# Performance work log

Hardware: AMD Instinct MI355X
Metric: run time of the kernel (lower is better)

## Reference

```python
import jax, jax.numpy as jnp
import numpy as np

THETA = 10000.0


def _rope(x, pos, theta):
    # x: [..., S, d_k] with d_k even; pos: [..., S] int positions
    d_k = x.shape[-1]
    inv_freq = 1.0 / (theta ** (jnp.arange(0, d_k, 2, dtype=jnp.float32) / d_k))  # [d_k/2]
    ang = pos[..., None].astype(jnp.float32) * inv_freq  # [..., S, d_k/2]
    cos, sin = jnp.cos(ang), jnp.sin(ang)
    x1 = x[..., 0::2]
    x2 = x[..., 1::2]
    r1 = x1 * cos - x2 * sin
    r2 = x1 * sin + x2 * cos
    # interleave back to [..., S, d_k]
    return jnp.stack([r1, r2], axis=-1).reshape(x.shape)


def setup_inputs() -> dict:
    key = jax.random.key(0)
    ks = jax.random.split(key, 5)
    B, S, D = 2, 2048, 1024
    scale = 0.02
    return {
        "in_features": jax.random.normal(ks[0], (B, S, D), dtype=jnp.float32),
        "q_proj": jax.random.normal(ks[1], (D, D), dtype=jnp.float32) * scale,
        "k_proj": jax.random.normal(ks[2], (D, D), dtype=jnp.float32) * scale,
        "v_proj": jax.random.normal(ks[3], (D, D), dtype=jnp.float32) * scale,
        "o_proj": jax.random.normal(ks[4], (D, D), dtype=jnp.float32) * scale,
    }


def reference(in_features, q_proj, k_proj, v_proj, o_proj):
    B, S, D = in_features.shape
    H = 16
    d_k = D // H
    pos = jnp.arange(S)  # broadcast over batch/heads

    def split_heads(x):  # [B,S,D] -> [B,H,S,d_k]
        return x.reshape(B, S, H, d_k).transpose(0, 2, 1, 3)

    Q = split_heads(in_features @ q_proj.T)
    K = split_heads(in_features @ k_proj.T)
    V = split_heads(in_features @ v_proj.T)

    Q = _rope(Q, pos, THETA)
    K = _rope(K, pos, THETA)

    scores = jnp.einsum("bhqd,bhkd->bhqk", Q, K) / jnp.sqrt(jnp.float32(d_k))
    causal = jnp.tril(jnp.ones((S, S), dtype=bool))
    scores = jnp.where(causal, scores, jnp.finfo(scores.dtype).min)
    attn = jax.nn.softmax(scores, axis=-1)
    out = jnp.einsum("bhqk,bhkd->bhqd", attn, V)  # [B,H,S,d_k]
    out = out.transpose(0, 2, 1, 3).reshape(B, S, D)
    return out @ o_proj.T
```

## Files before the change

kernel.cpp:

```cpp
#include <hip/hip_runtime.h>
#include <hip/hip_bf16.h>
#include <math.h>

#define Bdim 2
#define Sdim 2048
#define Ddim 1024
#define Hdim 16
#define DKdim 64
#define Mrows 4096

typedef __attribute__((ext_vector_type(8))) short bf16x8;
typedef __attribute__((ext_vector_type(4))) short short4v;
typedef __attribute__((ext_vector_type(4))) float f32x4;
typedef __attribute__((ext_vector_type(2))) unsigned int uint2v;

#define LOG2E_DIV8 0.18033688011112042f
#define NLOG2TH_64 0.20762050593046016f

__device__ __forceinline__ short f2bf(float f) {
  unsigned int x = __float_as_uint(f);
  x += 0x7fffu + ((x >> 16) & 1u);
  return (short)(x >> 16);
}

__device__ __forceinline__ float fast_exp2(float x) {
#if __has_builtin(__builtin_amdgcn_exp2f)
  return __builtin_amdgcn_exp2f(x);
#else
  return exp2f(x);
#endif
}

__device__ __forceinline__ unsigned int pack_bf2(float lo, float hi) {
  unsigned int r;
  asm("v_cvt_pk_bf16_f32 %0, %1, %2" : "=v"(r) : "v"(lo), "v"(hi));
  return r;
}

__device__ __forceinline__ void gl2lds16(const void* g, void* l) {
  __builtin_amdgcn_global_load_lds(
      (const __attribute__((address_space(1))) void*)g,
      (__attribute__((address_space(3))) void*)l, 16, 0, 0);
}

__global__ void cvt_kernel(const float* __restrict__ src, short* __restrict__ dst, int n) {
  int i = (blockIdx.x * blockDim.x + threadIdx.x) * 4;
  if (i + 3 < n) {
    float4 v = *(const float4*)(src + i);
    short4v o;
    o.x = f2bf(v.x); o.y = f2bf(v.y); o.z = f2bf(v.z); o.w = f2bf(v.w);
    *(short4v*)(dst + i) = o;
  }
}

__global__ void rope_tab_kernel(float2* __restrict__ T) {
  int idx = blockIdx.x * blockDim.x + threadIdx.x;
  int s = idx >> 5, f = idx & 31;
  float inv = exp2f(-NLOG2TH_64 * (float)(2 * f));
  float ang = (float)s * inv;
  float sn, cs;
  sincosf(ang, &sn, &cs);
  T[idx] = make_float2(sn, cs);
}

template<int MODE>
__global__ __launch_bounds__(256) void gemm_bt(
    const short* __restrict__ A, const short* __restrict__ Bw,
    float* __restrict__ Cf,
    short* __restrict__ Qout, short* __restrict__ Kout, short* __restrict__ Vout,
    const float2* __restrict__ RT,
    int Ndim, int Kdim)
{
  __shared__ __align__(16) short smem[17408];
  short (*st)[136] = (short(*)[136])smem;
  char* smemb = (char*)smem;

  const int tid  = threadIdx.x;
  const int lane = tid & 63;
  const int wid  = tid >> 6;
  const int wr = wid >> 1, wc = wid & 1;
  const int tile_m = blockIdx.x * 128;
  const int tile_n = blockIdx.y * 128;
  const int lrow = lane & 15;
  const int kgrp = lane >> 4;

  const int r0 = tid >> 2;
  const int sc = (tid & 3) * 8;
  const int lA0 = wid * 1024;
  const int lA1 = 4096  + wid * 1024;
  const int lB0 = 8192  + wid * 1024;
  const int lB1 = 12288 + wid * 1024;
  const short* gA0 = A  + (size_t)(tile_m + r0)      * Kdim + sc;
  const short* gA1 = A  + (size_t)(tile_m + r0 + 64) * Kdim + sc;
  const short* gB0 = Bw + (size_t)(tile_n + r0)      * Kdim + sc;
  const short* gB1 = Bw + (size_t)(tile_n + r0 + 64) * Kdim + sc;

  f32x4 acc[4][4];
#pragma unroll
  for (int i = 0; i < 4; i++)
#pragma unroll
    for (int j = 0; j < 4; j++) acc[i][j] = (f32x4)0.0f;

  for (int k0 = 0; k0 < Kdim; k0 += 32) {
    __syncthreads();
    gl2lds16(gA0 + k0, smemb + lA0);
    gl2lds16(gA1 + k0, smemb + lA1);
    gl2lds16(gB0 + k0, smemb + lB0);
    gl2lds16(gB1 + k0, smemb + lB1);
    __syncthreads();
    bf16x8 af[4], bfr[4];
#pragma unroll
    for (int i = 0; i < 4; i++)
      af[i]  = *(const bf16x8*)&smem[(wr*64 + i*16 + lrow)*32 + kgrp*8];
#pragma unroll
    for (int j = 0; j < 4; j++)
      bfr[j] = *(const bf16x8*)&smem[4096 + (wc*64 + j*16 + lrow)*32 + kgrp*8];
#pragma unroll
    for (int i = 0; i < 4; i++)
#pragma unroll
      for (int j = 0; j < 4; j++)
        acc[i][j] = __builtin_amdgcn_mfma_f32_16x16x32_bf16(af[i], bfr[j], acc[i][j], 0, 0, 0);
  }

  if (MODE == 0) {
#pragma unroll
    for (int i = 0; i < 4; i++)
#pragma unroll
      for (int j = 0; j < 4; j++)
#pragma unroll
        for (int r = 0; r < 4; r++) {
          int mr = tile_m + wr*64 + i*16 + kgrp*4 + r;
          int nc = tile_n + wc*64 + j*16 + lrow;
          Cf[(size_t)mr * Ndim + nc] = acc[i][j][r];
        }
  } else {
    const int sel = tile_n >> 10;
    __syncthreads();
#pragma unroll
    for (int i = 0; i < 4; i++)
#pragma unroll
      for (int j = 0; j < 4; j++)
#pragma unroll
        for (int r = 0; r < 4; r++) {
          float val   = acc[i][j][r];
          float other = __shfl_xor(val, 1, 64);
          int row = wr*64 + i*16 + kgrp*4 + r;
          int col = wc*64 + j*16 + lrow;
          short bv;
          if (sel == 2) {
            bv = f2bf(val);
          } else {
            int c = col & 63;
            int s = (tile_m + row) & 2047;
            float2 t = RT[(s << 5) + (c >> 1)];
            float rot = ((c & 1) == 0) ? (val * t.y - other * t.x)
                                       : (other * t.x + val * t.y);
            if (sel == 0) rot *= LOG2E_DIV8;
            bv = f2bf(rot);
          }
          st[row][col] = bv;
        }
    __syncthreads();
    if (sel < 2) {
      short* Out = (sel == 0) ? Qout : Kout;
#pragma unroll
      for (int p = 0; p < 8; p++) {
        int row = p*16 + (tid >> 4);
        int col = (tid & 15) * 8;
        bf16x8 v = *(const bf16x8*)&st[row][col];
        int mr = tile_m + row; int b = mr >> 11, s = mr & 2047;
        int nc = tile_n + col; int nn = nc & 1023;
        int h = nn >> 6, c = nn & 63;
        *(bf16x8*)&Out[((size_t)((b*Hdim + h)*Sdim + s))*DKdim + c] = v;
      }
    } else {
#pragma unroll
      for (int p = 0; p < 8; p++) {
        int col = p*16 + (tid >> 4);
        int sl  = (tid & 15) * 8;
        bf16x8 v;
#pragma unroll
        for (int e = 0; e < 8; e++) v[e] = st[sl + e][col];
        int nc = tile_n + col; int nn = nc & 1023;
        int h = nn >> 6, c = nn & 63;
        int m0 = tile_m + sl; int b = m0 >> 11, s0 = m0 & 2047;
        *(bf16x8*)&Vout[((size_t)((b*Hdim + h)*DKdim + c))*Sdim + s0] = v;
      }
    }
  }
}

__global__ __launch_bounds__(256, 2) void attn_kernel(
    const short* __restrict__ Q, const short* __restrict__ K,
    const short* __restrict__ Vt, short* __restrict__ O)
{
  const int bh = blockIdx.y;
  const int qt = (bh & 16) ? (int)blockIdx.x : (15 - (int)blockIdx.x);
  const int bq0 = qt * 128;
  const int tid  = threadIdx.x;
  const int wave = tid >> 6;
  const int lane = tid & 63;
  const int lrow = lane & 15, kgrp = lane >> 4;
  const short* Qb = Q  + (size_t)bh * Sdim * DKdim;
  const short* Kb = K  + (size_t)bh * Sdim * DKdim;
  const short* Vb = Vt + (size_t)bh * DKdim * Sdim;

  __shared__ __align__(16) char Kl[2][16384];
  __shared__ __align__(16) char Vl[2][16384];
  __shared__ __align__(16) char lPb[16384];

  const int q0w   = bq0 + wave*32;
  const int NT_w  = (q0w >> 6) + 1;
  const int NTP   = qt + 1;
  const int swz   = (lrow & 7) << 4;
  const int rowbase = wave*4096 + lrow*128;

  const int ldsoff = wave*4096 +  0;

  bf16x8 qf[2][2];
#pragma unroll
  for (int t = 0; t < 2; t++) {
    qf[t][0] = *(const bf16x8*)&Qb[(q0w + t*16 + lrow) * DKdim + kgrp*8];
    qf[t][1] = *(const bf16x8*)&Qb[(q0w + t*16 + lrow) * DKdim + 32 + kgrp*8];
  }

  f32x4 o[2][4];
  float psum[2] = {0.0f, 0.0f};
#pragma unroll
  for (int t = 0; t < 2; t++)
#pragma unroll
    for (int n = 0; n < 4; n++) o[t][n] = (f32x4)0.0f;

#pragma unroll
  for (int q = 0; q < 4; q++) {
    int c = wave*256 + q*64 + lane;
    int krow = c >> 3, kc16 = c & 7;
    gl2lds16((const char*)Kb + (size_t)krow * 128 + ((kc16*16) ^ ((krow & 7) << 4)),
             (char*)Kl[0] + ldsoff + q*1024);
    int vrow = c >> 4, vc16 = c & 15;
    gl2lds16((const char*)Vb + (size_t)vrow * (Sdim*2) + ((vc16*16) ^ ((vrow & 7) << 4)),
             (char*)Vl[0] + ldsoff + q*1024);
  }
  __syncthreads();

  int cur = 0;
  for (int it = 0; it < NTP; ++it) {
    const bool havenext = (it + 1 < NTP);
    if (havenext) {
      const int nkv = (it + 1) << 7;
      char* Kd = (char*)Kl[cur ^ 1] + ldsoff;
      char* Vd = (char*)Vl[cur ^ 1] + ldsoff;
#pragma unroll
      for (int q = 0; q < 4; q++) {
        int c = wave*256 + q*64 + lane;
        int krow = c >> 3, kc16 = c & 7;
        gl2lds16((const char*)Kb + (size_t)(nkv + krow) * 128 + ((kc16*16) ^ ((krow & 7) << 4)),
                 Kd + q*1024);
        int vrow = c >> 4, vc16 = c & 15;
        gl2lds16((const char*)Vb + (size_t)vrow * (Sdim*2) + nkv*2 + ((vc16*16) ^ ((vrow & 7) << 4)),
                 Vd + q*1024);
      }
    }
#pragma unroll
    for (int stt = 0; stt < 2; ++stt) {
      const int j = 2*it + stt;
      if (j < NT_w) {
        const int kv0 = j << 6;
        const char* Kc = Kl[cur] + stt*8192;
        const char* Vc = Vl[cur];
        const int vbo = stt*128;
        f32x4 sacc[2][4];
#pragma unroll
        for (int t = 0; t < 2; t++)
#pragma unroll
          for (int nch = 0; nch < 4; nch++) sacc[t][nch] = (f32x4)0.0f;
        __builtin_amdgcn_s_setprio(1);
#pragma unroll
        for (int nch = 0; nch < 4; nch++) {
          int rb = (nch*16 + lrow)*128;
          bf16x8 kf0 = *(const bf16x8*)(Kc + rb + ((kgrp*16) ^ swz));
          bf16x8 kf1 = *(const bf16x8*)(Kc + rb + ((kgrp*16 + 64) ^ swz));
          sacc[0][nch] = __builtin_amdgcn_mfma_f32_16x16x32_bf16(kf0, qf[0][0], sacc[0][nch], 0, 0, 0);
          sacc[0][nch] = __builtin_amdgcn_mfma_f32_16x16x32_bf16(kf1, qf[0][1], sacc[0][nch], 0, 0, 0);
          sacc[1][nch] = __builtin_amdgcn_mfma_f32_16x16x32_bf16(kf0, qf[1][0], sacc[1][nch], 0, 0, 0);
          sacc[1][nch] = __builtin_amdgcn_mfma_f32_16x16x32_bf16(kf1, qf[1][1], sacc[1][nch], 0, 0, 0);
        }
        __builtin_amdgcn_s_setprio(0);
        const bool diag = (j == NT_w - 1);
#pragma unroll
        for (int t = 0; t < 2; t++) {
          const int q_abs = q0w + t*16 + lrow;
#pragma unroll
          for (int nch = 0; nch < 4; nch++) {
            const int kbase = kv0 + nch*16 + kgrp*4;
            float p[4];
#pragma unroll
            for (int r = 0; r < 4; r++) {
              float e = fast_exp2(sacc[t][nch][r]);
              p[r] = (diag && (kbase + r > q_abs)) ? 0.0f : e;
            }
            psum[t] += (p[0] + p[1]) + (p[2] + p[3]);
            uint2v w;
            w.x = pack_bf2(p[0], p[1]);
            w.y = pack_bf2(p[2], p[3]);
            *(uint2v*)(lPb + rowbase + t*2048 + ((nch*32 + kgrp*8) ^ swz)) = w;
          }
        }
        asm volatile("s_waitcnt lgkmcnt(0)" ::: "memory");
        __builtin_amdgcn_sched_barrier(0);
        bf16x8 pa[2][2];
#pragma unroll
        for (int t = 0; t < 2; t++)
#pragma unroll
          for (int h = 0; h < 2; h++)
            pa[t][h] = *(const bf16x8*)(lPb + rowbase + t*2048 + ((h*64 + kgrp*16) ^ swz));
        __builtin_amdgcn_s_setprio(1);
#pragma unroll
        for (int n = 0; n < 4; n++) {
          int rb = (n*16 + lrow)*256 + vbo;
          bf16x8 vf0 = *(const bf16x8*)(Vc + rb + ((kgrp*16) ^ swz));
          bf16x8 vf1 = *(const bf16x8*)(Vc + rb + ((kgrp*16 + 64) ^ swz));
          o[0][n] = __builtin_amdgcn_mfma_f32_16x16x32_bf16(pa[0][0], vf0, o[0][n], 0, 0, 0);
          o[0][n] = __builtin_amdgcn_mfma_f32_16x16x32_bf16(pa[0][1], vf1, o[0][n], 0, 0, 0);
          o[1][n] = __builtin_amdgcn_mfma_f32_16x16x32_bf16(pa[1][0], vf0, o[1][n], 0, 0, 0);
          o[1][n] = __builtin_amdgcn_mfma_f32_16x16x32_bf16(pa[1][1], vf1, o[1][n], 0, 0, 0);
        }
        __builtin_amdgcn_s_setprio(0);
      }
    }
    __syncthreads();
    cur ^= 1;
  }

  float vt[2];
#pragma unroll
  for (int t = 0; t < 2; t++) {
    float v = psum[t];
    v += __shfl_xor(v, 16, 64);
    v += __shfl_xor(v, 32, 64);
    vt[t] = v;
  }
  const int hh = bh & 15, b = bh >> 4;
#pragma unroll
  for (int t = 0; t < 2; t++)
#pragma unroll
    for (int r = 0; r < 4; r++) {
      float rs = __frcp_rn(__shfl(vt[t], kgrp*4 + r, 64));
      int row = q0w + t*16 + kgrp*4 + r;
#pragma unroll
      for (int n = 0; n < 4; n++) {
        int col = hh*64 + n*16 + lrow;
        O[(size_t)(b*Sdim + row) * Ddim + col] = f2bf(o[t][n][r] * rs);
      }
    }
}

extern "C" void kernel_launch(void* const* d_in, const int* in_sizes, int n_in,
                              void* d_out, int out_size, void* d_ws, size_t ws_size,
                              hipStream_t stream) {
  const float* X  = (const float*)d_in[0];
  const float* Wq = (const float*)d_in[1];
  const float* Wk = (const float*)d_in[2];
  const float* Wv = (const float*)d_in[3];
  const float* Wo = (const float*)d_in[4];
  float* out = (float*)d_out;
  char* ws = (char*)d_ws;

  short* Xb   = (short*)(ws);
  short* Wqkv = (short*)(ws + 8388608);
  short* Wob  = (short*)(ws + 14680064);
  short* Qr   = (short*)(ws + 16777216);
  short* Kr   = (short*)(ws + 25165824);
  short* Vt   = (short*)(ws + 33554432);
  short* Ob   = (short*)(ws + 41943040);
  float2* RT  = (float2*)(ws + 41943040);

  const int DD = Ddim * Ddim;
  cvt_kernel<<<Mrows*Ddim/1024, 256, 0, stream>>>(X,  Xb,          Mrows*Ddim);
  cvt_kernel<<<DD/1024,         256, 0, stream>>>(Wq, Wqkv,        DD);
  cvt_kernel<<<DD/1024,         256, 0, stream>>>(Wk, Wqkv + DD,   DD);
  cvt_kernel<<<DD/1024,         256, 0, stream>>>(Wv, Wqkv + 2*DD, DD);
  cvt_kernel<<<DD/1024,         256, 0, stream>>>(Wo, Wob,         DD);
  rope_tab_kernel<<<Sdim*32/256, 256, 0, stream>>>(RT);

  gemm_bt<1><<<dim3(32, 24), 256, 0, stream>>>(Xb, Wqkv, (float*)nullptr,
                                               Qr, Kr, Vt, RT, 3072, 1024);
  attn_kernel<<<dim3(16, 32), 256, 0, stream>>>(Qr, Kr, Vt, Ob);
  gemm_bt<0><<<dim3(32, 8), 256, 0, stream>>>(Ob, Wob, out,
                                              nullptr, nullptr, nullptr, RT, 1024, 1024);
}
```

Measured before the change: 141.7 us.

## Double GEMM K-step to 64 and XOR-swizzle LDS tiles to avoid bank conflicts

```diff
diff --git a/kernel.cpp b/kernel.cpp
--- a/kernel.cpp
+++ b/kernel.cpp
@@ -84,16 +84,18 @@
   const int lrow = lane & 15;
   const int kgrp = lane >> 4;
 
-  const int r0 = tid >> 2;
-  const int sc = (tid & 3) * 8;
-  const int lA0 = wid * 1024;
-  const int lA1 = 4096  + wid * 1024;
-  const int lB0 = 8192  + wid * 1024;
-  const int lB1 = 12288 + wid * 1024;
-  const short* gA0 = A  + (size_t)(tile_m + r0)      * Kdim + sc;
-  const short* gA1 = A  + (size_t)(tile_m + r0 + 64) * Kdim + sc;
-  const short* gB0 = Bw + (size_t)(tile_n + r0)      * Kdim + sc;
-  const short* gB1 = Bw + (size_t)(tile_n + r0 + 64) * Kdim + sc;
+  const char* srcA[4];
+  const char* srcB[4];
+#pragma unroll
+  for (int i = 0; i < 4; i++) {
+    int c = i*256 + tid;
+    int row = c >> 3, q = c & 7;
+    int sw = (q*16) ^ ((row & 7) << 4);
+    srcA[i] = (const char*)(A  + (size_t)(tile_m + row) * Kdim) + sw;
+    srcB[i] = (const char*)(Bw + (size_t)(tile_n + row) * Kdim) + sw;
+  }
+  const int ldsA = wid * 1024;
+  const int ldsB = 16384 + wid * 1024;
 
   f32x4 acc[4][4];
 #pragma unroll
@@ -101,25 +103,33 @@
 #pragma unroll
     for (int j = 0; j < 4; j++) acc[i][j] = (f32x4)0.0f;
 
-  for (int k0 = 0; k0 < Kdim; k0 += 32) {
+  for (int k0 = 0; k0 < Kdim; k0 += 64) {
     __syncthreads();
-    gl2lds16(gA0 + k0, smemb + lA0);
-    gl2lds16(gA1 + k0, smemb + lA1);
-    gl2lds16(gB0 + k0, smemb + lB0);
-    gl2lds16(gB1 + k0, smemb + lB1);
+#pragma unroll
+    for (int i = 0; i < 4; i++) {
+      gl2lds16(srcA[i] + (size_t)k0*2, smemb + ldsA + i*4096);
+      gl2lds16(srcB[i] + (size_t)k0*2, smemb + 16384 + (ldsB - 16384) + i*4096);
+    }
     __syncthreads();
-    bf16x8 af[4], bfr[4];
-#pragma unroll
-    for (int i = 0; i < 4; i++)
-      af[i]  = *(const bf16x8*)&smem[(wr*64 + i*16 + lrow)*32 + kgrp*8];
-#pragma unroll
-    for (int j = 0; j < 4; j++)
-      bfr[j] = *(const bf16x8*)&smem[4096 + (wc*64 + j*16 + lrow)*32 + kgrp*8];
-#pragma unroll
-    for (int i = 0; i < 4; i++)
-#pragma unroll
-      for (int j = 0; j < 4; j++)
-        acc[i][j] = __builtin_amdgcn_mfma_f32_16x16x32_bf16(af[i], bfr[j], acc[i][j], 0, 0, 0);
+#pragma unroll
+    for (int ks = 0; ks < 2; ks++) {
+      bf16x8 af[4], bfr[4];
+#pragma unroll
+      for (int i = 0; i < 4; i++) {
+        int row = wr*64 + i*16 + lrow;
+        af[i] = *(const bf16x8*)(smemb + row*128 + ((ks*64 + kgrp*16) ^ ((row & 7) << 4)));
+      }
+#pragma unroll
+      for (int j = 0; j < 4; j++) {
+        int row = wc*64 + j*16 + lrow;
+        bfr[j] = *(const bf16x8*)(smemb + 16384 + row*128 + ((ks*64 + kgrp*16) ^ ((row & 7) << 4)));
+      }
+#pragma unroll
+      for (int i = 0; i < 4; i++)
+#pragma unroll
+        for (int j = 0; j < 4; j++)
+          acc[i][j] = __builtin_amdgcn_mfma_f32_16x16x32_bf16(af[i], bfr[j], acc[i][j], 0, 0, 0);
+    }
   }
 
   if (MODE == 0) {
@@ -215,7 +225,7 @@
   const int swz   = (lrow & 7) << 4;
   const int rowbase = wave*4096 + lrow*128;
 
-  const int ldsoff = wave*4096 +  0;
+  const int ldsoff = wave*4096;
 
   bf16x8 qf[2][2];
 #pragma unroll
```

Result: slower. 149.5 us (+5.5%).
